# Optimization experiments

Hardware: AMD Instinct MI355X
Metric: run time of the kernel (lower is better)

## Reference

```python
import jax, jax.numpy as jnp
import numpy as np

B, H, D, N, RPE = 4, 8, 64, 4096, 64
GAMMA = 0.999
N_LAYERS = 3
EPS = 1e-5


def _layernorm(x, w, b):
    mu = jnp.mean(x, axis=-1, keepdims=True)
    var = jnp.mean((x - mu) ** 2, axis=-1, keepdims=True)
    return (x - mu) / jnp.sqrt(var + EPS) * w + b


def _rpe(pos, pp_w, pp_b, ln_w, ln_b, lw, lb, oln_w, oln_b, out_w, out_b):
    # pos: [m, 1] scalar relative positions -> [h, m, d] Toeplitz kernel values
    x = pos @ pp_w + pp_b                       # [m, rpe_dim]
    for i in range(N_LAYERS):                   # residual=False path
        x = _layernorm(x, ln_w[i], ln_b[i])
        x = jax.nn.relu(x) @ lw[i] + lb[i]
    x = jax.nn.relu(_layernorm(x, oln_w, oln_b)) @ out_w + out_b  # [m, h*d]
    m = x.shape[0]
    return x.reshape(m, H, D).transpose(1, 0, 2)  # 'n (h d) -> h n d'


def setup_inputs() -> dict:
    key = jax.random.key(0)
    ks = jax.random.split(key, 4)
    x = jax.random.normal(ks[0], (B, H, N, D), dtype=jnp.float32)
    pp_w = jax.random.normal(ks[1], (1, RPE), dtype=jnp.float32) * 0.1
    pp_b = jnp.zeros((RPE,), dtype=jnp.float32)
    ln_w = jnp.ones((N_LAYERS, RPE), dtype=jnp.float32)
    ln_b = jnp.zeros((N_LAYERS, RPE), dtype=jnp.float32)
    lw = jax.random.normal(ks[2], (N_LAYERS, RPE, RPE), dtype=jnp.float32) * 0.1
    lb = jnp.zeros((N_LAYERS, RPE), dtype=jnp.float32)
    oln_w = jnp.ones((RPE,), dtype=jnp.float32)
    oln_b = jnp.zeros((RPE,), dtype=jnp.float32)
    out_w = jax.random.normal(ks[3], (RPE, H * D), dtype=jnp.float32) * 0.1
    out_b = jnp.zeros((H * D,), dtype=jnp.float32)
    return {"x": x, "pp_w": pp_w, "pp_b": pp_b, "ln_w": ln_w, "ln_b": ln_b,
            "lw": lw, "lb": lb, "oln_w": oln_w, "oln_b": oln_b,
            "out_w": out_w, "out_b": out_b}


def reference(x, pp_w, pp_b, ln_w, ln_b, lw, lb, oln_w, oln_b, out_w, out_b):
    # Tno.forward_fft, causal=True, use_decay=True, par_type=1
    rpe_args = (pp_w, pp_b, ln_w, ln_b, lw, lb, oln_w, oln_b, out_w, out_b)
    zero = _rpe(jnp.zeros((1, 1), dtype=x.dtype), *rpe_args)          # [h,1,d]
    pos_idx = jnp.arange(1, N, dtype=x.dtype).reshape(-1, 1)          # [n-1,1]
    pos = _rpe(pos_idx, *rpe_args)                                    # [h,n-1,d]
    coef = jnp.arange(1, N, dtype=x.dtype).reshape(1, -1, 1)
    pos = (GAMMA ** coef) * pos                                       # exp decay
    a = jax.nn.silu(jnp.concatenate([zero, pos, zero], axis=1))       # [h,n+1,d]
    # causal Toeplitz conv via length-2n FFT
    y = jnp.fft.rfft(x, 2 * N, axis=-2)                               # [b,h,n+1,d] cplx
    v = jnp.fft.rfft(a, 2 * N, axis=-2)[None]                         # [1,h,n+1,d]
    out = jnp.fft.irfft(v * y, 2 * N, axis=-2)[:, :, :N, :]
    return out
```

## Files before the change

kernel.cpp:

```cpp
#include <hip/hip_runtime.h>
#include <math.h>

#define NSEQ 4096
#define MFT  4096
#define CHX  2048
#define CHA  512

#define LP2 4224
static __device__ __forceinline__ int pf(int i) { return i + (i >> 5); }

static __device__ __forceinline__ float wsum64(float v) {
    v += __shfl_xor(v, 1);
    v += __shfl_xor(v, 2);
    v += __shfl_xor(v, 4);
    v += __shfl_xor(v, 8);
    v += __shfl_xor(v, 16);
    v += __shfl_xor(v, 32);
    return v;
}

static __device__ __forceinline__ void ln_pair(float& x0, float& x1, float w, float b) {
    float mu0 = wsum64(x0) * (1.0f / 64.0f);
    float mu1 = wsum64(x1) * (1.0f / 64.0f);
    float d0 = x0 - mu0, d1 = x1 - mu1;
    float v0 = wsum64(d0 * d0) * (1.0f / 64.0f);
    float v1 = wsum64(d1 * d1) * (1.0f / 64.0f);
    x0 = d0 * rsqrtf(v0 + 1e-5f) * w + b;
    x1 = d1 * rsqrtf(v1 + 1e-5f) * w + b;
}

__global__ __launch_bounds__(256) void k_pre(
    const float* __restrict__ x,
    const float* __restrict__ pp_w, const float* __restrict__ pp_b,
    const float* __restrict__ ln_w, const float* __restrict__ ln_b,
    const float* __restrict__ lw,   const float* __restrict__ lb,
    const float* __restrict__ oln_w,const float* __restrict__ oln_b,
    const float* __restrict__ out_w,const float* __restrict__ out_b,
    float* __restrict__ xT, float* __restrict__ aT)
{
    __shared__ float tile[64][65];
    const int t = threadIdx.x;

    if (blockIdx.x >= 512) {
        const int bid = blockIdx.x - 512;
        const int slab = bid >> 6;
        const int r0 = (bid & 63) * 64;
        const size_t base = (size_t)slab * 262144u;
        const int tc = t & 63, t4 = t >> 6;
        const float* s = x + base + (size_t)r0 * 64;
#pragma unroll
        for (int k = 0; k < 16; ++k) {
            int rr = t4 + k * 4;
            tile[rr][tc] = s[rr * 64 + tc];
        }
        __syncthreads();
        float* d = xT + base + r0;
#pragma unroll
        for (int k = 0; k < 16; ++k) {
            int cc = t4 + k * 4;
            d[(size_t)cc * 4096 + tc] = tile[tc][cc];
        }
        return;
    }

    const int wave = t >> 6;
    const int lane = t & 63;
    const int mbase = ((int)blockIdx.x * 4 + wave) * 2;
    const float m0 = (float)mbase, m1 = (float)(mbase + 1);

    float x0 = fmaf(m0, pp_w[lane], pp_b[lane]);
    float x1 = fmaf(m1, pp_w[lane], pp_b[lane]);

    for (int L = 0; L < 3; ++L) {
        ln_pair(x0, x1, ln_w[L * 64 + lane], ln_b[L * 64 + lane]);
        float r0 = fmaxf(x0, 0.0f), r1 = fmaxf(x1, 0.0f);
        float y0 = lb[L * 64 + lane], y1 = y0;
        const float* W = lw + L * 4096;
#pragma unroll 8
        for (int i = 0; i < 64; ++i) {
            float wi = W[i * 64 + lane];
            y0 = fmaf(__shfl(r0, i), wi, y0);
            y1 = fmaf(__shfl(r1, i), wi, y1);
        }
        x0 = y0; x1 = y1;
    }
    ln_pair(x0, x1, oln_w[lane], oln_b[lane]);
    float r0 = fmaxf(x0, 0.0f), r1 = fmaxf(x1, 0.0f);

    float acc0[8], acc1[8];
#pragma unroll
    for (int k = 0; k < 8; ++k) {
        float ob = out_b[k * 64 + lane];
        acc0[k] = ob; acc1[k] = ob;
    }
#pragma unroll 4
    for (int i = 0; i < 64; ++i) {
        float a0 = __shfl(r0, i);
        float a1 = __shfl(r1, i);
        const float* Wr = out_w + i * 512;
#pragma unroll
        for (int k = 0; k < 8; ++k) {
            float wv = Wr[k * 64 + lane];
            acc0[k] = fmaf(a0, wv, acc0[k]);
            acc1[k] = fmaf(a1, wv, acc1[k]);
        }
    }
    const float LOGG = -0.0010005003335835335f;
    float d0 = __expf(m0 * LOGG);
    float d1 = __expf(m1 * LOGG);
#pragma unroll
    for (int k = 0; k < 8; ++k) {
        int c = k * 64 + lane;
        float2 o;
        float v;
        v = acc0[k] * d0; o.x = v / (1.0f + __expf(-v));
        v = acc1[k] * d1; o.y = v / (1.0f + __expf(-v));
        *(float2*)(aT + (size_t)c * 4096 + mbase) = o;
    }
}

__global__ __launch_bounds__(256) void k_transpose(const float* __restrict__ src,
                                                   float* __restrict__ dst,
                                                   int R, int C) {
    __shared__ float tile[64][65];
    size_t slab = (size_t)blockIdx.z * (size_t)R * (size_t)C;
    int c0 = blockIdx.x * 64, r0 = blockIdx.y * 64;
    int t = threadIdx.x;
    int tc = t & 63, t4 = t >> 6;
    const float* s = src + slab + (size_t)r0 * C + c0;
#pragma unroll
    for (int k = 0; k < 16; ++k) {
        int rr = t4 + k * 4;
        tile[rr][tc] = s[(size_t)rr * C + tc];
    }
    __syncthreads();
    float* d = dst + slab + (size_t)c0 * R + r0;
#pragma unroll
    for (int k = 0; k < 16; ++k) {
        int cc = t4 + k * 4;
        d[(size_t)cc * R + tc] = tile[tc][cc];
    }
}

static __device__ __forceinline__ void cmulrw(float& r, float& i, float wr, float wi) {
    float t = r * wr - i * wi;
    i = r * wi + i * wr;
    r = t;
}

template<bool INV>
static __device__ __forceinline__ void dft4(float& ar, float& ai, float& br, float& bi,
                                            float& cr, float& ci, float& dr, float& di) {
    float t0r = ar + cr, t0i = ai + ci, t1r = ar - cr, t1i = ai - ci;
    float t2r = br + dr, t2i = bi + di, t3r = br - dr, t3i = bi - di;
    float u3r = INV ? -t3i : t3i;
    float u3i = INV ?  t3r : -t3r;
    ar = t0r + t2r; ai = t0i + t2i;
    br = t1r + u3r; bi = t1i + u3i;
    cr = t0r - t2r; ci = t0i - t2i;
    dr = t1r - u3r; di = t1i - u3i;
}

template<bool INV>
static __device__ __forceinline__ void radix16(float (&vr)[16], float (&vi)[16]) {
    const float C1 = 0.92387953251128674f;
    const float S1 = 0.38268343236508978f;
    const float R2 = 0.70710678118654752f;
    const float SG = INV ? 1.0f : -1.0f;
#pragma unroll
    for (int na = 0; na < 4; ++na)
        dft4<INV>(vr[na], vi[na], vr[na + 4], vi[na + 4],
                  vr[na + 8], vi[na + 8], vr[na + 12], vi[na + 12]);
    cmulrw(vr[5],  vi[5],   C1, SG * S1);
    cmulrw(vr[9],  vi[9],   R2, SG * R2);
    cmulrw(vr[13], vi[13],  S1, SG * C1);
    cmulrw(vr[6],  vi[6],   R2, SG * R2);
    {
        float tmp = vr[10];
        if (INV) { vr[10] = -vi[10]; vi[10] =  tmp; }
        else     { vr[10] =  vi[10]; vi[10] = -tmp; }
    }
    cmulrw(vr[14], vi[14], -R2, SG * R2);
    cmulrw(vr[7],  vi[7],   S1, SG * C1);
    cmulrw(vr[11], vi[11], -R2, SG * R2);
    cmulrw(vr[15], vi[15], -C1, -SG * S1);
    float yr[16], yi[16];
#pragma unroll
    for (int kb = 0; kb < 4; ++kb) {
        float ar = vr[4*kb+0], ai = vi[4*kb+0], br = vr[4*kb+1], bi = vi[4*kb+1];
        float cr = vr[4*kb+2], ci = vi[4*kb+2], dr = vr[4*kb+3], di = vi[4*kb+3];
        dft4<INV>(ar, ai, br, bi, cr, ci, dr, di);
        yr[kb]      = ar; yi[kb]      = ai;
        yr[kb + 4]  = br; yi[kb + 4]  = bi;
        yr[kb + 8]  = cr; yi[kb + 8]  = ci;
        yr[kb + 12] = dr; yi[kb + 12] = di;
    }
#pragma unroll
    for (int k = 0; k < 16; ++k) { vr[k] = yr[k]; vi[k] = yi[k]; }
}

template<bool INV>
static __device__ __forceinline__ void fft4096_reg(float (&vr)[16], float (&vi)[16],
                                                   float2* __restrict__ lds, int t)
{
    radix16<INV>(vr, vi);
    __syncthreads();
#pragma unroll
    for (int k3 = 0; k3 < 16; ++k3)
        lds[pf(t + (k3 << 8))] = make_float2(vr[k3], vi[k3]);
    __syncthreads();
    {
        int n1 = t & 15, k3 = t >> 4;
        float ang = (float)k3 * (1.0f / 128.0f);
        float wr = cospif(ang);
        float wi = INV ? sinpif(ang) : -sinpif(ang);
        float cr = 1.0f, ci = 0.0f;
#pragma unroll
        for (int n2 = 0; n2 < 16; ++n2) {
            float2 v = lds[pf(n1 + (n2 << 4) + (k3 << 8))];
            vr[n2] = v.x * cr - v.y * ci;
            vi[n2] = v.x * ci + v.y * cr;
            float ncr = cr * wr - ci * wi;
            ci = cr * wi + ci * wr; cr = ncr;
        }
    }
    radix16<INV>(vr, vi);
    __syncthreads();
#pragma unroll
    for (int k2 = 0; k2 < 16; ++k2)
        lds[pf(t + (k2 << 8))] = make_float2(vr[k2], vi[k2]);
    __syncthreads();
    {
        float ang = (float)t * (1.0f / 2048.0f);
        float wr = cospif(ang);
        float wi = INV ? sinpif(ang) : -sinpif(ang);
        float cr = 1.0f, ci = 0.0f;
#pragma unroll
        for (int n1 = 0; n1 < 16; ++n1) {
            float2 v = lds[pf((t << 4) + n1)];
            vr[n1] = v.x * cr - v.y * ci;
            vi[n1] = v.x * ci + v.y * cr;
            float ncr = cr * wr - ci * wi;
            ci = cr * wi + ci * wr; cr = ncr;
        }
    }
    radix16<INV>(vr, vi);
}

__global__ __launch_bounds__(256, 4) void k_fft_fwd(const float2* __restrict__ src,
                                                    float2* __restrict__ dst) {
    __shared__ float2 lds[LP2];
    const int t = threadIdx.x;
    const float2* s = src + (size_t)blockIdx.x * 2048;
    float vr[16], vi[16];
#pragma unroll
    for (int n3 = 0; n3 < 8; ++n3) {
        float2 v = s[t + (n3 << 8)];
        vr[n3] = v.x; vi[n3] = v.y;
    }
#pragma unroll
    for (int n3 = 8; n3 < 16; ++n3) { vr[n3] = 0.0f; vi[n3] = 0.0f; }
    fft4096_reg<false>(vr, vi, lds, t);
    float2* d = dst + (size_t)blockIdx.x * 4096;
#pragma unroll
    for (int k1 = 0; k1 < 16; ++k1)
        d[t + (k1 << 8)] = make_float2(vr[k1], vi[k1]);
}

__global__ __launch_bounds__(256, 4) void k_fft_conv_inv(const float2* __restrict__ xrow,
                                                         const float2* __restrict__ Za,
                                                         float* __restrict__ yT) {
    __shared__ float2 lds[LP2];
    const int t = threadIdx.x;
    const int bc = blockIdx.x;
    const int ca = bc & 511;
    const float2* s = xrow + (size_t)bc * 2048;
    float vr[16], vi[16];
#pragma unroll
    for (int n3 = 0; n3 < 8; ++n3) {
        float2 v = s[t + (n3 << 8)];
        vr[n3] = v.x; vi[n3] = v.y;
    }
#pragma unroll
    for (int n3 = 8; n3 < 16; ++n3) { vr[n3] = 0.0f; vi[n3] = 0.0f; }
    fft4096_reg<false>(vr, vi, lds, t);

    __syncthreads();
#pragma unroll
    for (int k1 = 0; k1 < 16; ++k1)
        lds[pf(t + (k1 << 8))] = make_float2(vr[k1], vi[k1]);
    __syncthreads();

    const float2* za = Za + (size_t)ca * 4096;
    for (int f = t; f <= 2048; f += 256) {
        const int fm = (4096 - f) & 4095;
        float2 Xf = lds[pf(f)], Xm = lds[pf(fm)];
        float2 Af = za[f], Am = za[fm];
        float Exr = 0.5f * (Xf.x + Xm.x), Exi = 0.5f * (Xf.y - Xm.y);
        float Oxr = 0.5f * (Xf.y + Xm.y), Oxi = 0.5f * (Xm.x - Xf.x);
        float Ear = 0.5f * (Af.x + Am.x), Eai = 0.5f * (Af.y - Am.y);
        float Oar = 0.5f * (Af.y + Am.y), Oai = 0.5f * (Am.x - Af.x);
        float fr = (float)f * (1.0f / 4096.0f);
        float cp = cospif(fr), sp = sinpif(fr);
        float tOxr = cp * Oxr + sp * Oxi, tOxi = cp * Oxi - sp * Oxr;
        float tOar = cp * Oar + sp * Oai, tOai = cp * Oai - sp * Oar;
        float Xpr = Exr + tOxr, Xpi = Exi + tOxi;
        float Xqr = Exr - tOxr, Xqi = Exi - tOxi;
        float Apr = Ear + tOar, Api = Eai + tOai;
        float Aqr = Ear - tOar, Aqi = Eai - tOai;
        float Pr = Xpr * Apr - Xpi * Api, Pi = Xpr * Api + Xpi * Apr;
        float Qr = Xqr * Aqr - Xqi * Aqi, Qi = Xqr * Aqi + Xqi * Aqr;
        float Sr = 0.5f * (Pr + Qr), Si = 0.5f * (Pi + Qi);
        float Dr = 0.5f * (Pr - Qr), Di = 0.5f * (Pi - Qi);
        float Cr = cp * Dr - sp * Di, Ci = cp * Di + sp * Dr;
        lds[pf(f)]  = make_float2(Sr - Ci, Si + Cr);
        lds[pf(fm)] = make_float2(Sr + Ci, Cr - Si);
    }
    __syncthreads();
#pragma unroll
    for (int n3 = 0; n3 < 16; ++n3) {
        float2 v = lds[pf(t + (n3 << 8))];
        vr[n3] = v.x; vi[n3] = v.y;
    }
    fft4096_reg<true>(vr, vi, lds, t);

    const float sc = 1.0f / 4096.0f;
    float2* dst = (float2*)yT + (size_t)bc * 2048;
#pragma unroll
    for (int k1 = 0; k1 < 8; ++k1) {
        int idx = t + (k1 << 8);
        dst[idx] = make_float2(vr[k1] * sc, vi[k1] * sc);
    }
}

extern "C" void kernel_launch(void* const* d_in, const int* in_sizes, int n_in,
                              void* d_out, int out_size, void* d_ws, size_t ws_size,
                              hipStream_t stream) {
    const float* x     = (const float*)d_in[0];
    const float* pp_w  = (const float*)d_in[1];
    const float* pp_b  = (const float*)d_in[2];
    const float* ln_w  = (const float*)d_in[3];
    const float* ln_b  = (const float*)d_in[4];
    const float* lw    = (const float*)d_in[5];
    const float* lb    = (const float*)d_in[6];
    const float* oln_w = (const float*)d_in[7];
    const float* oln_b = (const float*)d_in[8];
    const float* out_w = (const float*)d_in[9];
    const float* out_b = (const float*)d_in[10];
    float* out = (float*)d_out;
    char* ws = (char*)d_ws;

    float*  xT = (float*)(ws);
    float*  aT = (float*)(ws + 33554432u);
    float2* Za = (float2*)(ws + 41943040u);
    float*  yT = xT;

    k_pre<<<2560, 256, 0, stream>>>(x, pp_w, pp_b, ln_w, ln_b, lw, lb,
                                    oln_w, oln_b, out_w, out_b, xT, aT);
    k_fft_fwd<<<CHA, 256, 0, stream>>>((const float2*)aT, Za);
    k_fft_conv_inv<<<CHX, 256, 0, stream>>>((const float2*)xT, Za, yT);
    k_transpose<<<dim3(64, 1, 32), 256, 0, stream>>>(yT, out, 64, 4096);
}
```

Measured before the change: 179.3 us.

## Precompute unpacked kernel spectra and twiddle table, switch LDS padding to XOR swizzle

The forward FFT kernel now does the real-FFT even/odd unpacking of the decay-kernel spectrum once and stores both half-spectrum values as a float4 per frequency. It also writes a cospi/sinpi table from one extra block. The conv kernel therefore reads one contiguous float4 plus the table instead of two scattered float2 loads and trig calls, and it no longer repeats the unpack work for every batch. LDS padding is replaced by an XOR swizzle so the shared array shrinks to 4096 entries, which allows launch bounds of 5 blocks per SM. The risks are swizzle bank conflicts on some access patterns and the larger workspace needed for the unpacked rows.

```diff
diff --git a/kernel.cpp b/kernel.cpp
--- a/kernel.cpp
+++ b/kernel.cpp
@@ -6,8 +6,7 @@
 #define CHX  2048
 #define CHA  512
 
-#define LP2 4224
-static __device__ __forceinline__ int pf(int i) { return i + (i >> 5); }
+static __device__ __forceinline__ int sf(int i) { return i ^ ((i >> 4) & 15); }
 
 static __device__ __forceinline__ float wsum64(float v) {
     v += __shfl_xor(v, 1);
@@ -207,7 +206,7 @@
     __syncthreads();
 #pragma unroll
     for (int k3 = 0; k3 < 16; ++k3)
-        lds[pf(t + (k3 << 8))] = make_float2(vr[k3], vi[k3]);
+        lds[sf(t + (k3 << 8))] = make_float2(vr[k3], vi[k3]);
     __syncthreads();
     {
         int n1 = t & 15, k3 = t >> 4;
@@ -217,7 +216,7 @@
         float cr = 1.0f, ci = 0.0f;
 #pragma unroll
         for (int n2 = 0; n2 < 16; ++n2) {
-            float2 v = lds[pf(n1 + (n2 << 4) + (k3 << 8))];
+            float2 v = lds[sf(n1 + (n2 << 4) + (k3 << 8))];
             vr[n2] = v.x * cr - v.y * ci;
             vi[n2] = v.x * ci + v.y * cr;
             float ncr = cr * wr - ci * wi;
@@ -228,7 +227,7 @@
     __syncthreads();
 #pragma unroll
     for (int k2 = 0; k2 < 16; ++k2)
-        lds[pf(t + (k2 << 8))] = make_float2(vr[k2], vi[k2]);
+        lds[sf(t + (k2 << 8))] = make_float2(vr[k2], vi[k2]);
     __syncthreads();
     {
         float ang = (float)t * (1.0f / 2048.0f);
@@ -237,7 +236,7 @@
         float cr = 1.0f, ci = 0.0f;
 #pragma unroll
         for (int n1 = 0; n1 < 16; ++n1) {
-            float2 v = lds[pf((t << 4) + n1)];
+            float2 v = lds[sf((t << 4) + n1)];
             vr[n1] = v.x * cr - v.y * ci;
             vi[n1] = v.x * ci + v.y * cr;
             float ncr = cr * wr - ci * wi;
@@ -247,10 +246,19 @@
     radix16<INV>(vr, vi);
 }
 
-__global__ __launch_bounds__(256, 4) void k_fft_fwd(const float2* __restrict__ src,
-                                                    float2* __restrict__ dst) {
-    __shared__ float2 lds[LP2];
+#define ZAROW 4100
+__global__ __launch_bounds__(256, 5) void k_fft_fwd(const float2* __restrict__ src,
+                                                    float2* __restrict__ ZaU,
+                                                    float2* __restrict__ ctab) {
+    __shared__ float2 lds[4096];
     const int t = threadIdx.x;
+    if (blockIdx.x == CHA) {
+        for (int f = t; f <= 2048; f += 256) {
+            float fr = (float)f * (1.0f / 4096.0f);
+            ctab[f] = make_float2(cospif(fr), sinpif(fr));
+        }
+        return;
+    }
     const float2* s = src + (size_t)blockIdx.x * 2048;
     float vr[16], vi[16];
 #pragma unroll
@@ -261,16 +269,34 @@
 #pragma unroll
     for (int n3 = 8; n3 < 16; ++n3) { vr[n3] = 0.0f; vi[n3] = 0.0f; }
     fft4096_reg<false>(vr, vi, lds, t);
-    float2* d = dst + (size_t)blockIdx.x * 4096;
+
+    __syncthreads();
 #pragma unroll
     for (int k1 = 0; k1 < 16; ++k1)
-        d[t + (k1 << 8)] = make_float2(vr[k1], vi[k1]);
-}
-
-__global__ __launch_bounds__(256, 4) void k_fft_conv_inv(const float2* __restrict__ xrow,
-                                                         const float2* __restrict__ Za,
+        lds[sf(t + (k1 << 8))] = make_float2(vr[k1], vi[k1]);
+    __syncthreads();
+
+    float4* zu = (float4*)(ZaU + (size_t)blockIdx.x * ZAROW);
+    for (int f = t; f <= 2048; f += 256) {
+        const int fm = (4096 - f) & 4095;
+        float2 Zf = lds[sf(f)], Zm = lds[sf(fm)];
+        float Ear = 0.5f * (Zf.x + Zm.x), Eai = 0.5f * (Zf.y - Zm.y);
+        float Oar = 0.5f * (Zf.y + Zm.y), Oai = 0.5f * (Zm.x - Zf.x);
+        float fr = (float)f * (1.0f / 4096.0f);
+        float cp = cospif(fr), sp = sinpif(fr);
+        float tOr = cp * Oar + sp * Oai, tOi = cp * Oai - sp * Oar;
+        float4 o;
+        o.x = Ear + tOr; o.y = Eai + tOi;
+        o.z = Ear - tOr; o.w = Eai - tOi;
+        zu[f] = o;
+    }
+}
+
+__global__ __launch_bounds__(256, 5) void k_fft_conv_inv(const float2* __restrict__ xrow,
+                                                         const float2* __restrict__ ZaU,
+                                                         const float2* __restrict__ ctab,
                                                          float* __restrict__ yT) {
-    __shared__ float2 lds[LP2];
+    __shared__ float2 lds[4096];
     const int t = threadIdx.x;
     const int bc = blockIdx.x;
     const int ca = bc & 511;
@@ -288,38 +314,33 @@
     __syncthreads();
 #pragma unroll
     for (int k1 = 0; k1 < 16; ++k1)
-        lds[pf(t + (k1 << 8))] = make_float2(vr[k1], vi[k1]);
-    __syncthreads();
-
-    const float2* za = Za + (size_t)ca * 4096;
+        lds[sf(t + (k1 << 8))] = make_float2(vr[k1], vi[k1]);
+    __syncthreads();
+
+    const float4* zu = (const float4*)(ZaU + (size_t)ca * ZAROW);
     for (int f = t; f <= 2048; f += 256) {
         const int fm = (4096 - f) & 4095;
-        float2 Xf = lds[pf(f)], Xm = lds[pf(fm)];
-        float2 Af = za[f], Am = za[fm];
+        float2 Xf = lds[sf(f)], Xm = lds[sf(fm)];
+        float4 A = zu[f];
+        float2 ct = ctab[f];
+        float cp = ct.x, sp = ct.y;
         float Exr = 0.5f * (Xf.x + Xm.x), Exi = 0.5f * (Xf.y - Xm.y);
         float Oxr = 0.5f * (Xf.y + Xm.y), Oxi = 0.5f * (Xm.x - Xf.x);
-        float Ear = 0.5f * (Af.x + Am.x), Eai = 0.5f * (Af.y - Am.y);
-        float Oar = 0.5f * (Af.y + Am.y), Oai = 0.5f * (Am.x - Af.x);
-        float fr = (float)f * (1.0f / 4096.0f);
-        float cp = cospif(fr), sp = sinpif(fr);
         float tOxr = cp * Oxr + sp * Oxi, tOxi = cp * Oxi - sp * Oxr;
-        float tOar = cp * Oar + sp * Oai, tOai = cp * Oai - sp * Oar;
         float Xpr = Exr + tOxr, Xpi = Exi + tOxi;
         float Xqr = Exr - tOxr, Xqi = Exi - tOxi;
-        float Apr = Ear + tOar, Api = Eai + tOai;
-        float Aqr = Ear - tOar, Aqi = Eai - tOai;
-        float Pr = Xpr * Apr - Xpi * Api, Pi = Xpr * Api + Xpi * Apr;
-        float Qr = Xqr * Aqr - Xqi * Aqi, Qi = Xqr * Aqi + Xqi * Aqr;
+        float Pr = Xpr * A.x - Xpi * A.y, Pi = Xpr * A.y + Xpi * A.x;
+        float Qr = Xqr * A.z - Xqi * A.w, Qi = Xqr * A.w + Xqi * A.z;
         float Sr = 0.5f * (Pr + Qr), Si = 0.5f * (Pi + Qi);
         float Dr = 0.5f * (Pr - Qr), Di = 0.5f * (Pi - Qi);
         float Cr = cp * Dr - sp * Di, Ci = cp * Di + sp * Dr;
-        lds[pf(f)]  = make_float2(Sr - Ci, Si + Cr);
-        lds[pf(fm)] = make_float2(Sr + Ci, Cr - Si);
+        lds[sf(f)]  = make_float2(Sr - Ci, Si + Cr);
+        lds[sf(fm)] = make_float2(Sr + Ci, Cr - Si);
     }
     __syncthreads();
 #pragma unroll
     for (int n3 = 0; n3 < 16; ++n3) {
-        float2 v = lds[pf(t + (n3 << 8))];
+        float2 v = lds[sf(t + (n3 << 8))];
         vr[n3] = v.x; vi[n3] = v.y;
     }
     fft4096_reg<true>(vr, vi, lds, t);
@@ -350,14 +371,15 @@
     float* out = (float*)d_out;
     char* ws = (char*)d_ws;
 
-    float*  xT = (float*)(ws);
-    float*  aT = (float*)(ws + 33554432u);
-    float2* Za = (float2*)(ws + 41943040u);
-    float*  yT = xT;
+    float*  xT   = (float*)(ws);
+    float*  aT   = (float*)(ws + 33554432u);
+    float2* ZaU  = (float2*)(ws + 41943040u);
+    float2* ctab = (float2*)(ws + 58736640u);
+    float*  yT   = xT;
 
     k_pre<<<2560, 256, 0, stream>>>(x, pp_w, pp_b, ln_w, ln_b, lw, lb,
                                     oln_w, oln_b, out_w, out_b, xT, aT);
-    k_fft_fwd<<<CHA, 256, 0, stream>>>((const float2*)aT, Za);
-    k_fft_conv_inv<<<CHX, 256, 0, stream>>>((const float2*)xT, Za, yT);
+    k_fft_fwd<<<CHA + 1, 256, 0, stream>>>((const float2*)aT, ZaU, ctab);
+    k_fft_conv_inv<<<CHX, 256, 0, stream>>>((const float2*)xT, ZaU, ctab, yT);
     k_transpose<<<dim3(64, 1, 32), 256, 0, stream>>>(yT, out, 64, 4096);
 }
```

New measurement: 204.1 us. 1.14x slower.
